# Performance work log

Measured on AMD Instinct MI355X. Metric: run time of the kernel, lower is better.

## Reference

```python
import jax, jax.numpy as jnp
import numpy as np

N_NODES = 512
N_VEC = 8          # n_vectors_hidden
N_FEAT = 128       # n_invariant_feat_hidden
MLP_UNITS = [128, 128]


def _mlp(x, Ws):
    # e3nn-style MLP on scalars: no bias, weights scaled by 1/sqrt(fan_in), silu on every layer
    for W in Ws:
        x = jax.nn.silu(x @ W / jnp.sqrt(jnp.asarray(W.shape[0], x.dtype)))
    return x


def setup_inputs() -> dict:
    key = jax.random.key(0)
    ks = jax.random.split(key, 12)
    d_edge = N_VEC + 2 * N_FEAT  # 264
    inp = {
        "positions": jax.random.normal(ks[0], (N_NODES, N_VEC, 3), jnp.float32),
        "features": jax.random.normal(ks[1], (N_NODES, N_FEAT), jnp.float32),
        # phi_e
        "We1": jax.random.normal(ks[2], (d_edge, MLP_UNITS[0]), jnp.float32),
        "We2": jax.random.normal(ks[3], (MLP_UNITS[0], MLP_UNITS[1]), jnp.float32),
        # phi_x
        "Wx1": jax.random.normal(ks[4], (MLP_UNITS[1], MLP_UNITS[0]), jnp.float32),
        "Wx2": jax.random.normal(ks[5], (MLP_UNITS[0], MLP_UNITS[1]), jnp.float32),
        # phi_inf
        "Winf": jax.random.normal(ks[6], (MLP_UNITS[1], 1), jnp.float32),
        # FullyConnectedTensorProduct weights: [scalar_mul, sh_mul, out_mul]
        "Wtp": jax.random.normal(ks[7], (MLP_UNITS[1], N_VEC, N_VEC), jnp.float32),
        # phi_h + final linear
        "Wh1": jax.random.normal(ks[8], (MLP_UNITS[1] + N_FEAT, MLP_UNITS[0]), jnp.float32),
        "Wh2": jax.random.normal(ks[9], (MLP_UNITS[0], MLP_UNITS[1]), jnp.float32),
        "Wh3": jax.random.normal(ks[10], (MLP_UNITS[1], N_FEAT), jnp.float32),
    }
    return inp


def reference(positions, features, We1, We2, Wx1, Wx2, Winf, Wtp, Wh1, Wh2, Wh3):
    n, V, _ = positions.shape
    # fully-connected edge list (senders sorted, self-loops excluded)
    idx = np.arange(n)
    senders = np.repeat(idx, n - 1)                                  # [E]
    receivers = (senders + np.tile(np.arange(1, n), n)) % n          # [E]

    vectors = positions[senders] - positions[receivers]              # [E,V,3]
    sq = jnp.sum(vectors * vectors, axis=-1)
    lengths = jnp.sqrt(jnp.maximum(sq, 1e-20))                       # safe_norm [E,V]

    edge_feat = jnp.concatenate(
        [lengths, features[senders], features[receivers]], axis=-1)  # [E, V+2F]
    m_ij = _mlp(edge_feat, [We1, We2])                               # [E, U]
    phi_x_out = _mlp(m_ij, [Wx1, Wx2])                               # [E, U]

    unit = vectors / lengths[..., None]                              # [E,V,3]
    sh1 = jnp.sqrt(jnp.asarray(3.0, unit.dtype)) * unit              # ell=1, component norm
    # FCTP: only 0e (x) 1o -> 1o path reaches the n_vectors x 1o output
    U = phi_x_out.shape[-1]
    norm = jnp.sqrt(jnp.asarray(U * V, sh1.dtype))
    out_vec = jnp.einsum('uvw,eu,evk->ewk', Wtp, phi_x_out, sh1) / norm  # [E,W,3]

    vector_per_node = jax.ops.segment_sum(out_vec, senders, num_segments=n)  # [n,W,3]

    e = jax.nn.sigmoid(m_ij @ Winf / jnp.sqrt(jnp.asarray(Winf.shape[0], m_ij.dtype)))  # [E,1]
    m_i = jax.ops.segment_sum(m_ij * e, senders, num_segments=n)     # [n,U]

    h = _mlp(jnp.concatenate([m_i, features], axis=-1), [Wh1, Wh2])
    h = h @ Wh3 / jnp.sqrt(jnp.asarray(Wh3.shape[0], h.dtype))       # final linear -> F
    features_out = h + features                                      # residual_h
    positions_out = positions + vector_per_node
    return positions_out, features_out
```

## Files before the change

kernel.cpp:

```cpp
#include <hip/hip_runtime.h>
#include <math.h>

#define NN   512
#define NV   8
#define CH   32
#define NCHH 8

#define C1 0.06154574548966636f
#define C2 0.08838834764831845f
#define SQRT3 1.7320508075688772f

typedef __attribute__((ext_vector_type(8))) short bf16x8;
typedef __attribute__((ext_vector_type(4))) float f32x4;

#define MFMA16 __builtin_amdgcn_mfma_f32_16x16x32_bf16
#define CVT_PK(dst, a, b) asm("v_cvt_pk_bf16_f32 %0, %1, %2" : "=v"(dst) : "v"(a), "v"(b))

__device__ __forceinline__ float silu_f(float x) {
    float e = __builtin_amdgcn_exp2f(x * -1.442695041f);
    return x * __builtin_amdgcn_rcpf(1.0f + e);
}
__device__ __forceinline__ float sigm_f(float x) {
    float e = __builtin_amdgcn_exp2f(x * -1.442695041f);
    return __builtin_amdgcn_rcpf(1.0f + e);
}
__device__ __forceinline__ short f2bf(float f) {
    unsigned u = __builtin_bit_cast(unsigned, f);
    u = (u + 0x7FFFu + ((u >> 16) & 1u)) >> 16;
    return (short)u;
}
__device__ __forceinline__ float bfhi(unsigned u) {
    return __builtin_bit_cast(float, u & 0xFFFF0000u);
}
__device__ __forceinline__ float bflo(unsigned u) {
    return __builtin_bit_cast(float, u << 16);
}

__device__ __forceinline__ void packW(const float* __restrict__ W,
                                      short* __restrict__ out, int ncols, int ct,
                                      float scale)
{
    int t = threadIdx.x;
    int lane = t & 63, kt = (t >> 6) & 3;
    int g = lane >> 4, c = lane & 15;
    bf16x8 v;
    #pragma unroll
    for (int j = 0; j < 8; ++j)
        v[j] = f2bf(W[(kt * 32 + g * 8 + j) * ncols + ct * 16 + c] * scale);
    *(bf16x8*)(out + (size_t)(ct * 256 + t) * 8) = v;
}

__global__ __launch_bounds__(256)
void k_packall(const float* __restrict__ We2, const float* __restrict__ Wx1,
               const float* __restrict__ Wx2, const float* __restrict__ Wtp,
               const float* __restrict__ We1, const float* __restrict__ feat,
               short* __restrict__ We2p, short* __restrict__ Wx1p,
               short* __restrict__ Wx2p, short* __restrict__ Wtpp,
               short* __restrict__ We1Lp,
               float* __restrict__ FsP, float* __restrict__ FrP)
{
    const int b = blockIdx.x, t = threadIdx.x;
    if (b < 8)  { packW(We2, We2p, 128, b,      C2);       return; }
    if (b < 16) { packW(Wx1, Wx1p, 128, b - 8,  C2);       return; }
    if (b < 24) { packW(Wx2, Wx2p, 128, b - 16, C2);       return; }
    if (b < 28) { packW(Wtp, Wtpp,  64, b - 24, 0.03125f); return; }
    if (b == 28) {
        #pragma unroll
        for (int h = 0; h < 2; ++h) {
            int tt = t + h * 256;
            int ct = tt >> 6, l = tt & 63, g = l >> 4, c = l & 15;
            bf16x8 v = {0,0,0,0,0,0,0,0};
            if (g == 0) {
                #pragma unroll
                for (int j = 0; j < 8; ++j)
                    v[j] = f2bf(We1[j * 128 + ct * 16 + c] * C1);
            }
            *(bf16x8*)(We1Lp + (size_t)tt * 8) = v;
        }
        return;
    }
    __shared__ float sF[256];
    const int n = (b - 29) * 2 + (t >> 7), j = t & 127, hb = t & 128;
    sF[t] = feat[n * 128 + j];
    __syncthreads();
    float a = 0.f, bb = 0.f;
    #pragma unroll 8
    for (int k = 0; k < 128; ++k) {
        float f = sF[hb + k];
        a  = fmaf(f, We1[(8   + k) * 128 + j], a);
        bb = fmaf(f, We1[(136 + k) * 128 + j], bb);
    }
    FsP[n * 128 + j] = a * C1;
    FrP[n * 128 + j] = bb * C1;
}

__device__ __forceinline__ void loadBz(const short* __restrict__ p,
                                       bf16x8 (&B)[2][4], int w, int lane)
{
    int zz = 0; asm volatile("" : "+v"(zz));
    const bf16x8* p8 = (const bf16x8*)p;
    #pragma unroll
    for (int ctl = 0; ctl < 2; ++ctl)
        #pragma unroll
        for (int kt = 0; kt < 4; ++kt)
            B[ctl][kt] = p8[((w * 2 + ctl) * 4 + kt) * 64 + lane + zz];
}

__device__ __forceinline__ void gemm_mfma(const short* sIn_, const bf16x8 (&B)[2][4],
                                          const int (&adrK)[4], f32x4 (&acc)[2][2])
{
    const char* sIn = (const char*)sIn_;
    const f32x4 z = {0.f, 0.f, 0.f, 0.f};
    acc[0][0] = z; acc[0][1] = z; acc[1][0] = z; acc[1][1] = z;
    __builtin_amdgcn_s_setprio(1);
    #pragma unroll
    for (int kt = 0; kt < 4; ++kt) {
        bf16x8 a0 = *(const bf16x8*)(sIn + adrK[kt]);
        bf16x8 a1 = *(const bf16x8*)(sIn + adrK[kt] + 4096);
        acc[0][0] = MFMA16(a0, B[0][kt], acc[0][0], 0, 0, 0);
        acc[0][1] = MFMA16(a0, B[1][kt], acc[0][1], 0, 0, 0);
        acc[1][0] = MFMA16(a1, B[0][kt], acc[1][0], 0, 0, 0);
        acc[1][1] = MFMA16(a1, B[1][kt], acc[1][1], 0, 0, 0);
    }
    __builtin_amdgcn_s_setprio(0);
}

template<bool KEEP>
__device__ __forceinline__ void epi_store(const f32x4 (&acc)[2][2], short* sOut_,
                                          const int (&wAdr)[2][4], f32x4 (&keep)[2][2])
{
    char* sOut = (char*)sOut_;
    #pragma unroll
    for (int rt = 0; rt < 2; ++rt)
        #pragma unroll
        for (int ctl = 0; ctl < 2; ++ctl) {
            float v0 = silu_f(acc[rt][ctl][0]);
            float v1 = silu_f(acc[rt][ctl][1]);
            float v2 = silu_f(acc[rt][ctl][2]);
            float v3 = silu_f(acc[rt][ctl][3]);
            if (KEEP) {
                keep[rt][ctl][0] = v0; keep[rt][ctl][1] = v1;
                keep[rt][ctl][2] = v2; keep[rt][ctl][3] = v3;
            }
            unsigned p01, p23;
            CVT_PK(p01, v0, v1);
            CVT_PK(p23, v2, v3);
            char* o = sOut + rt * 4096;
            *(short*)(o + wAdr[ctl][0]) = (short)(p01 & 0xFFFFu);
            *(short*)(o + wAdr[ctl][1]) = (short)(p01 >> 16);
            *(short*)(o + wAdr[ctl][2]) = (short)(p23 & 0xFFFFu);
            *(short*)(o + wAdr[ctl][3]) = (short)(p23 >> 16);
        }
}

__global__ __launch_bounds__(256, 4)
void k_edge(const float* __restrict__ pos,
            const float* __restrict__ Winf,
            const float* __restrict__ FsP,
            const float* __restrict__ FrP,
            const short* __restrict__ We1Lp,
            const short* __restrict__ We2p,
            const short* __restrict__ Wx1p,
            const short* __restrict__ Wx2p,
            const short* __restrict__ Wtpp,
            float* __restrict__ MI2,
            float* __restrict__ VEC2)
{
    __shared__ __align__(16) short sX[CH * 128];
    __shared__ __align__(16) short sY[CH * 128];
    __shared__ __align__(16) float sLS[CH * NV * 4];
    __shared__ float sWinf[8 * 17];
    __shared__ float sPosS[24];
    __shared__ float sE[CH];
    __shared__ float sVp[4 * 24];

    const int bid = blockIdx.x;
    const int s = bid >> 1, half = bid & 1;
    const int t = threadIdx.x;
    const int lane = t & 63, w = t >> 6;
    const int rl = lane & 15, kg = lane >> 4;

    const int swz = (rl & 7) << 4;
    const int ktperm = (rl & 4) << 4;
    const int baseRd = rl * 256 + ((kg * 16) ^ (swz & 0x30));
    int adrK[4];
    #pragma unroll
    for (int kt = 0; kt < 4; ++kt) adrK[kt] = baseRd + ((kt * 64) ^ ktperm);
    int wAdr[2][4];
    #pragma unroll
    for (int ctl = 0; ctl < 2; ++ctl)
        #pragma unroll
        for (int jj = 0; jj < 4; ++jj) {
            int r = kg * 4 + jj;
            wAdr[ctl][jj] = r * 256 + ((w * 64 + ctl * 32 + 2 * rl) ^ ((r & 7) << 4));
        }
    const int colg0 = w * 32 + rl, colg1 = colg0 + 16;
    const int er = t >> 3, eo = t & 7;
    const int eAdr0 = er * 256 + ((eo * 32)      ^ ((er & 7) << 4));
    const int eAdr1 = er * 256 + ((eo * 32 + 16) ^ ((er & 7) << 4));
    const int vv = w * 2 + (rl >> 3);

    if (t < 128) sWinf[(t >> 4) * 17 + (t & 15)] = Winf[t];
    if (t < 24)  sPosS[t] = pos[s * 24 + t];

    const float fs0 = FsP[s * 128 + colg0];
    const float fs1 = FsP[s * 128 + colg1];

    float miacc0 = 0.f, miacc1 = 0.f;
    float vax = 0.f, vay = 0.f, vaz = 0.f;
    __syncthreads();

    for (int c = 0; c < NCHH; ++c) {
        const int r0 = (half * NCHH + c) * CH;

        bf16x8 Bw[2][4];
        loadBz(We2p, Bw, w, lane);
        bf16x8 bL0, bL1;
        {
            int zz = 0; asm volatile("" : "+v"(zz));
            const bf16x8* pL = (const bf16x8*)We1Lp;
            bL0 = pL[(w * 2 + 0) * 64 + lane + zz];
            bL1 = pL[(w * 2 + 1) * 64 + lane + zz];
        }
        f32x4 cIn[2][2];
        {
            int zz = 0; asm volatile("" : "+v"(zz));
            #pragma unroll
            for (int rt = 0; rt < 2; ++rt)
                #pragma unroll
                for (int jj = 0; jj < 4; ++jj) {
                    const float* fp = FrP + (size_t)(r0 + rt * 16 + kg * 4 + jj) * 128 + zz;
                    cIn[rt][0][jj] = fp[colg0] + fs0;
                    cIn[rt][1][jj] = fp[colg1] + fs1;
                }
        }

        {
            int r = t >> 3, v = t & 7;
            const float* pr = pos + (size_t)(r0 + r) * 24 + v * 3;
            float dx = sPosS[v * 3 + 0] - pr[0];
            float dy = sPosS[v * 3 + 1] - pr[1];
            float dz = sPosS[v * 3 + 2] - pr[2];
            float sq = fmaxf(dx * dx + dy * dy + dz * dz, 1e-20f);
            float rs = __builtin_amdgcn_rsqf(sq);
            float len = sq * rs;
            float inv = SQRT3 * rs;
            f32x4 o; o[0] = dx * inv; o[1] = dy * inv; o[2] = dz * inv; o[3] = len;
            *(f32x4*)(sLS + (r * 8 + (v ^ (r & 7))) * 4) = o;
        }
        __syncthreads();

        {
            bf16x8 aL0 = {0,0,0,0,0,0,0,0}, aL1 = {0,0,0,0,0,0,0,0};
            if (kg == 0) {
                const float* Lp = sLS + rl * 32;
                const float* Lq = sLS + (rl + 16) * 32;
                unsigned u0[4], u1[4];
                #pragma unroll
                for (int jp = 0; jp < 4; ++jp) {
                    CVT_PK(u0[jp], Lp[((2*jp)   ^ (rl & 7)) * 4 + 3],
                                   Lp[((2*jp+1) ^ (rl & 7)) * 4 + 3]);
                    CVT_PK(u1[jp], Lq[((2*jp)   ^ (rl & 7)) * 4 + 3],
                                   Lq[((2*jp+1) ^ (rl & 7)) * 4 + 3]);
                }
                uint4 v0 = {u0[0], u0[1], u0[2], u0[3]};
                uint4 v1 = {u1[0], u1[1], u1[2], u1[3]};
                aL0 = __builtin_bit_cast(bf16x8, v0);
                aL1 = __builtin_bit_cast(bf16x8, v1);
            }
            f32x4 aP[2][2];
            aP[0][0] = MFMA16(aL0, bL0, cIn[0][0], 0, 0, 0);
            aP[0][1] = MFMA16(aL0, bL1, cIn[0][1], 0, 0, 0);
            aP[1][0] = MFMA16(aL1, bL0, cIn[1][0], 0, 0, 0);
            aP[1][1] = MFMA16(aL1, bL1, cIn[1][1], 0, 0, 0);
            f32x4 dummy[2][2];
            epi_store<false>(aP, sX, wAdr, dummy);
        }
        __syncthreads();

        f32x4 acc[2][2];
        f32x4 keepM[2][2];
        gemm_mfma(sX, Bw, adrK, acc);
        bf16x8 Bn[2][4];
        loadBz(Wx1p, Bn, w, lane);
        epi_store<true>(acc, sY, wAdr, keepM);
        __syncthreads();

        {
            const char* sYc = (const char*)sY;
            uint4 m0 = *(const uint4*)(sYc + eAdr0);
            uint4 m1 = *(const uint4*)(sYc + eAdr1);
            const unsigned mu[8] = {m0.x, m0.y, m0.z, m0.w, m1.x, m1.y, m1.z, m1.w};
            float d = 0.f;
            #pragma unroll
            for (int q = 0; q < 8; ++q) {
                d = fmaf(bflo(mu[q]), sWinf[eo * 17 + 2 * q],     d);
                d = fmaf(bfhi(mu[q]), sWinf[eo * 17 + 2 * q + 1], d);
            }
            d += __shfl_xor(d, 1); d += __shfl_xor(d, 2); d += __shfl_xor(d, 4);
            if (eo == 0) sE[er] = (r0 + er == s) ? 0.f : sigm_f(d * C2);
        }
        __syncthreads();

        #pragma unroll
        for (int rt = 0; rt < 2; ++rt)
            #pragma unroll
            for (int jj = 0; jj < 4; ++jj) {
                float e = sE[rt * 16 + kg * 4 + jj];
                miacc0 = fmaf(keepM[rt][0][jj], e, miacc0);
                miacc1 = fmaf(keepM[rt][1][jj], e, miacc1);
            }

        gemm_mfma(sY, Bn, adrK, acc);
        loadBz(Wx2p, Bw, w, lane);
        epi_store<false>(acc, sX, wAdr, keepM);
        __syncthreads();

        gemm_mfma(sX, Bw, adrK, acc);
        bf16x8 Bt[4];
        {
            int zz = 0; asm volatile("" : "+v"(zz));
            const bf16x8* p8 = (const bf16x8*)Wtpp;
            #pragma unroll
            for (int kt = 0; kt < 4; ++kt) Bt[kt] = p8[(w * 4 + kt) * 64 + lane + zz];
        }
        epi_store<false>(acc, sY, wAdr, keepM);
        __syncthreads();

        {
            const f32x4 z = {0.f, 0.f, 0.f, 0.f};
            f32x4 acc0 = z, acc1 = z;
            const char* sYc = (const char*)sY;
            __builtin_amdgcn_s_setprio(1);
            #pragma unroll
            for (int kt = 0; kt < 4; ++kt) {
                bf16x8 a0 = *(const bf16x8*)(sYc + adrK[kt]);
                bf16x8 a1 = *(const bf16x8*)(sYc + adrK[kt] + 4096);
                acc0 = MFMA16(a0, Bt[kt], acc0, 0, 0, 0);
                acc1 = MFMA16(a1, Bt[kt], acc1, 0, 0, 0);
            }
            __builtin_amdgcn_s_setprio(0);
            #pragma unroll
            for (int rt = 0; rt < 2; ++rt)
                #pragma unroll
                for (int jj = 0; jj < 4; ++jj) {
                    int row = rt * 16 + kg * 4 + jj;
                    const f32x4 sh = *(const f32x4*)(sLS + (row * 8 + (vv ^ (row & 7))) * 4);
                    float g = rt ? acc1[jj] : acc0[jj];
                    vax = fmaf(g, sh[0], vax);
                    vay = fmaf(g, sh[1], vay);
                    vaz = fmaf(g, sh[2], vaz);
                }
        }
        __syncthreads();
    }

    miacc0 += __shfl_xor(miacc0, 16); miacc0 += __shfl_xor(miacc0, 32);
    miacc1 += __shfl_xor(miacc1, 16); miacc1 += __shfl_xor(miacc1, 32);
    if (lane < 16) {
        float* mo = MI2 + (size_t)(half * NN + s) * 128;
        mo[w * 32 + lane]      = miacc0;
        mo[w * 32 + 16 + lane] = miacc1;
    }
    vax += __shfl_xor(vax, 8);  vay += __shfl_xor(vay, 8);  vaz += __shfl_xor(vaz, 8);
    vax += __shfl_xor(vax, 16); vay += __shfl_xor(vay, 16); vaz += __shfl_xor(vaz, 16);
    vax += __shfl_xor(vax, 32); vay += __shfl_xor(vay, 32); vaz += __shfl_xor(vaz, 32);
    if ((lane & 56) == 0) {
        float* vp = sVp + w * 24 + lane * 3;
        vp[0] = vax; vp[1] = vay; vp[2] = vaz;
    }
    __syncthreads();
    if (t < 24) {
        float sum = sVp[t] + sVp[24 + t] + sVp[48 + t] + sVp[72 + t];
        VEC2[(size_t)(half * NN + s) * 24 + t] = sum;
    }
}

__global__ __launch_bounds__(128)
void k_node(const float* __restrict__ pos, const float* __restrict__ feat,
            const float* __restrict__ Wh1, const float* __restrict__ Wh2,
            const float* __restrict__ Wh3,
            const float* __restrict__ MI2, const float* __restrict__ VEC2,
            float* __restrict__ outPos, float* __restrict__ outFeat)
{
    __shared__ float sMi[128], sF[128], sH[128];
    int n = blockIdx.x, j = threadIdx.x;
    sMi[j] = MI2[n * 128 + j] + MI2[NN * 128 + n * 128 + j];
    sF[j]  = feat[n * 128 + j];
    __syncthreads();
    float a = 0.f;
    #pragma unroll 8
    for (int k = 0; k < 128; ++k) a = fmaf(sMi[k], Wh1[k * 128 + j], a);
    #pragma unroll 8
    for (int k = 0; k < 128; ++k) a = fmaf(sF[k], Wh1[(128 + k) * 128 + j], a);
    a = silu_f(a * 0.0625f);
    sH[j] = a;
    __syncthreads();
    float b = 0.f;
    #pragma unroll 8
    for (int k = 0; k < 128; ++k) b = fmaf(sH[k], Wh2[k * 128 + j], b);
    b = silu_f(b * C2);
    sMi[j] = b;
    __syncthreads();
    float cc = 0.f;
    #pragma unroll 8
    for (int k = 0; k < 128; ++k) cc = fmaf(sMi[k], Wh3[k * 128 + j], cc);
    outFeat[n * 128 + j] = cc * C2 + sF[j];
    if (j < 24) outPos[n * 24 + j] = pos[n * 24 + j]
                                   + VEC2[n * 24 + j] + VEC2[NN * 24 + n * 24 + j];
}

extern "C" void kernel_launch(void* const* d_in, const int* in_sizes, int n_in,
                              void* d_out, int out_size, void* d_ws, size_t ws_size,
                              hipStream_t stream) {
    const float* pos  = (const float*)d_in[0];
    const float* feat = (const float*)d_in[1];
    const float* We1  = (const float*)d_in[2];
    const float* We2  = (const float*)d_in[3];
    const float* Wx1  = (const float*)d_in[4];
    const float* Wx2  = (const float*)d_in[5];
    const float* Winf = (const float*)d_in[6];
    const float* Wtp  = (const float*)d_in[7];
    const float* Wh1  = (const float*)d_in[8];
    const float* Wh2  = (const float*)d_in[9];
    const float* Wh3  = (const float*)d_in[10];

    float* outPos  = (float*)d_out;
    float* outFeat = (float*)d_out + NN * 24;

    float* ws   = (float*)d_ws;
    float* FsP  = ws;
    float* FrP  = ws + 65536;
    float* MI2  = ws + 131072;
    float* VEC2 = ws + 262144;
    short* wpack = (short*)(ws + 286720);
    short* We2p  = wpack;
    short* Wx1p  = wpack + 16384;
    short* Wx2p  = wpack + 32768;
    short* Wtpp  = wpack + 49152;
    short* We1Lp = wpack + 57344;

    k_packall<<<dim3(285), dim3(256), 0, stream>>>(We2, Wx1, Wx2, Wtp, We1, feat,
                                                   We2p, Wx1p, Wx2p, Wtpp, We1Lp,
                                                   FsP, FrP);
    k_edge<<<dim3(2 * NN), dim3(256), 0, stream>>>(pos, Winf, FsP, FrP, We1Lp,
                                                   We2p, Wx1p, Wx2p, Wtpp, MI2, VEC2);
    k_node<<<dim3(NN), dim3(128), 0, stream>>>(pos, feat, Wh1, Wh2, Wh3, MI2, VEC2,
                                               outPos, outFeat);
}
```

Baseline: 94.97 us.

## Double-buffer edge geometry and prefetch next chunk to drop barriers

Edge geometry (unit vectors and lengths) now sits in a double-buffered shared array. The next chunk's geometry is computed during the current chunk's phi_x stage instead of at the top of each iteration, which removes that iteration's barrier. The first phi_x GEMM and its epilogue move before the barrier that publishes the attention weights, and the barrier at the end of the loop is dropped, leaving fewer block-wide syncs per chunk. The cost is extra shared memory and registers for the sender positions, plus more reliance on the remaining barriers to order the shared-buffer reuse correctly.

```diff
diff --git a/kernel.cpp b/kernel.cpp
--- a/kernel.cpp
+++ b/kernel.cpp
@@ -168,9 +168,8 @@
 {
     __shared__ __align__(16) short sX[CH * 128];
     __shared__ __align__(16) short sY[CH * 128];
-    __shared__ __align__(16) float sLS[CH * NV * 4];
+    __shared__ __align__(16) float sLS[2][CH * NV * 4];
     __shared__ float sWinf[8 * 17];
-    __shared__ float sPosS[24];
     __shared__ float sE[CH];
     __shared__ float sVp[4 * 24];
 
@@ -201,17 +200,36 @@
     const int vv = w * 2 + (rl >> 3);
 
     if (t < 128) sWinf[(t >> 4) * 17 + (t & 15)] = Winf[t];
-    if (t < 24)  sPosS[t] = pos[s * 24 + t];
 
     const float fs0 = FsP[s * 128 + colg0];
     const float fs1 = FsP[s * 128 + colg1];
 
+    const int p0r = t >> 3, p0v = t & 7;
+    const int p0off = (p0r * 8 + (p0v ^ (p0r & 7))) * 4;
+    const float psx = pos[s * 24 + p0v * 3 + 0];
+    const float psy = pos[s * 24 + p0v * 3 + 1];
+    const float psz = pos[s * 24 + p0v * 3 + 2];
+
     float miacc0 = 0.f, miacc1 = 0.f;
     float vax = 0.f, vay = 0.f, vaz = 0.f;
+
+    {
+        int row = ((half * NCHH) * CH + p0r) & 511;
+        const float* pr = pos + (size_t)row * 24 + p0v * 3;
+        float dx = psx - pr[0], dy = psy - pr[1], dz = psz - pr[2];
+        float sq = fmaxf(dx * dx + dy * dy + dz * dz, 1e-20f);
+        float rs = __builtin_amdgcn_rsqf(sq);
+        float len = sq * rs;
+        float inv = SQRT3 * rs;
+        f32x4 o; o[0] = dx * inv; o[1] = dy * inv; o[2] = dz * inv; o[3] = len;
+        *(f32x4*)(sLS[0] + p0off) = o;
+    }
     __syncthreads();
 
     for (int c = 0; c < NCHH; ++c) {
         const int r0 = (half * NCHH + c) * CH;
+        const float* lsCur = sLS[c & 1];
+        float* lsNxt = sLS[(c + 1) & 1];
 
         bf16x8 Bw[2][4];
         loadBz(We2p, Bw, w, lane);
@@ -236,25 +254,10 @@
         }
 
         {
-            int r = t >> 3, v = t & 7;
-            const float* pr = pos + (size_t)(r0 + r) * 24 + v * 3;
-            float dx = sPosS[v * 3 + 0] - pr[0];
-            float dy = sPosS[v * 3 + 1] - pr[1];
-            float dz = sPosS[v * 3 + 2] - pr[2];
-            float sq = fmaxf(dx * dx + dy * dy + dz * dz, 1e-20f);
-            float rs = __builtin_amdgcn_rsqf(sq);
-            float len = sq * rs;
-            float inv = SQRT3 * rs;
-            f32x4 o; o[0] = dx * inv; o[1] = dy * inv; o[2] = dz * inv; o[3] = len;
-            *(f32x4*)(sLS + (r * 8 + (v ^ (r & 7))) * 4) = o;
-        }
-        __syncthreads();
-
-        {
             bf16x8 aL0 = {0,0,0,0,0,0,0,0}, aL1 = {0,0,0,0,0,0,0,0};
             if (kg == 0) {
-                const float* Lp = sLS + rl * 32;
-                const float* Lq = sLS + (rl + 16) * 32;
+                const float* Lp = lsCur + rl * 32;
+                const float* Lq = lsCur + (rl + 16) * 32;
                 unsigned u0[4], u1[4];
                 #pragma unroll
                 for (int jp = 0; jp < 4; ++jp) {
@@ -300,6 +303,10 @@
             d += __shfl_xor(d, 1); d += __shfl_xor(d, 2); d += __shfl_xor(d, 4);
             if (eo == 0) sE[er] = (r0 + er == s) ? 0.f : sigm_f(d * C2);
         }
+
+        gemm_mfma(sY, Bn, adrK, acc);
+        loadBz(Wx2p, Bw, w, lane);
+        epi_store<false>(acc, sX, wAdr, keepM);
         __syncthreads();
 
         #pragma unroll
@@ -311,11 +318,6 @@
                 miacc1 = fmaf(keepM[rt][1][jj], e, miacc1);
             }
 
-        gemm_mfma(sY, Bn, adrK, acc);
-        loadBz(Wx2p, Bw, w, lane);
-        epi_store<false>(acc, sX, wAdr, keepM);
-        __syncthreads();
-
         gemm_mfma(sX, Bw, adrK, acc);
         bf16x8 Bt[4];
         {
@@ -323,6 +325,17 @@
             const bf16x8* p8 = (const bf16x8*)Wtpp;
             #pragma unroll
             for (int kt = 0; kt < 4; ++kt) Bt[kt] = p8[(w * 4 + kt) * 64 + lane + zz];
+        }
+        {
+            int row = (r0 + CH + p0r) & 511;
+            const float* pr = pos + (size_t)row * 24 + p0v * 3;
+            float dx = psx - pr[0], dy = psy - pr[1], dz = psz - pr[2];
+            float sq = fmaxf(dx * dx + dy * dy + dz * dz, 1e-20f);
+            float rs = __builtin_amdgcn_rsqf(sq);
+            float len = sq * rs;
+            float inv = SQRT3 * rs;
+            f32x4 o; o[0] = dx * inv; o[1] = dy * inv; o[2] = dz * inv; o[3] = len;
+            *(f32x4*)(lsNxt + p0off) = o;
         }
         epi_store<false>(acc, sY, wAdr, keepM);
         __syncthreads();
@@ -345,14 +358,13 @@
                 #pragma unroll
                 for (int jj = 0; jj < 4; ++jj) {
                     int row = rt * 16 + kg * 4 + jj;
-                    const f32x4 sh = *(const f32x4*)(sLS + (row * 8 + (vv ^ (row & 7))) * 4);
+                    const f32x4 sh = *(const f32x4*)(lsCur + (row * 8 + (vv ^ (row & 7))) * 4);
                     float g = rt ? acc1[jj] : acc0[jj];
                     vax = fmaf(g, sh[0], vax);
                     vay = fmaf(g, sh[1], vay);
                     vaz = fmaf(g, sh[2], vaz);
                 }
         }
-        __syncthreads();
     }
 
     miacc0 += __shfl_xor(miacc0, 16); miacc0 += __shfl_xor(miacc0, 32);
```

New measurement: 96.52 us. Within noise of the previous version (+1.6%).

## Double edge-kernel block to 512 threads with 16-column tiles per wave

Applied to the files above, without the earlier changes.

The edge kernel now uses 8 waves per block instead of 4. Each wave computes 16 output columns instead of 32, which halves per-thread MFMA accumulators and weight registers. The goal is more waves in flight to hide latency and shorter serial per-wave chains. In exchange there are more barrier participants, each weight fragment is loaded by more waves, and the final TP GEMM runs on only half the waves.

```diff
diff --git a/kernel.cpp b/kernel.cpp
--- a/kernel.cpp
+++ b/kernel.cpp
@@ -94,66 +94,60 @@
     FrP[n * 128 + j] = bb * C1;
 }
 
-__device__ __forceinline__ void loadBz(const short* __restrict__ p,
-                                       bf16x8 (&B)[2][4], int w, int lane)
+__device__ __forceinline__ void loadB16(const short* __restrict__ p,
+                                        bf16x8 (&B)[4], int w, int lane)
 {
     int zz = 0; asm volatile("" : "+v"(zz));
     const bf16x8* p8 = (const bf16x8*)p;
     #pragma unroll
-    for (int ctl = 0; ctl < 2; ++ctl)
-        #pragma unroll
-        for (int kt = 0; kt < 4; ++kt)
-            B[ctl][kt] = p8[((w * 2 + ctl) * 4 + kt) * 64 + lane + zz];
-}
-
-__device__ __forceinline__ void gemm_mfma(const short* sIn_, const bf16x8 (&B)[2][4],
-                                          const int (&adrK)[4], f32x4 (&acc)[2][2])
+    for (int kt = 0; kt < 4; ++kt)
+        B[kt] = p8[(w * 4 + kt) * 64 + lane + zz];
+}
+
+__device__ __forceinline__ void gemm16(const short* sIn_, const bf16x8 (&B)[4],
+                                       const int (&adrK)[4], f32x4 (&acc)[2])
 {
     const char* sIn = (const char*)sIn_;
     const f32x4 z = {0.f, 0.f, 0.f, 0.f};
-    acc[0][0] = z; acc[0][1] = z; acc[1][0] = z; acc[1][1] = z;
+    acc[0] = z; acc[1] = z;
     __builtin_amdgcn_s_setprio(1);
     #pragma unroll
     for (int kt = 0; kt < 4; ++kt) {
         bf16x8 a0 = *(const bf16x8*)(sIn + adrK[kt]);
         bf16x8 a1 = *(const bf16x8*)(sIn + adrK[kt] + 4096);
-        acc[0][0] = MFMA16(a0, B[0][kt], acc[0][0], 0, 0, 0);
-        acc[0][1] = MFMA16(a0, B[1][kt], acc[0][1], 0, 0, 0);
-        acc[1][0] = MFMA16(a1, B[0][kt], acc[1][0], 0, 0, 0);
-        acc[1][1] = MFMA16(a1, B[1][kt], acc[1][1], 0, 0, 0);
+        acc[0] = MFMA16(a0, B[kt], acc[0], 0, 0, 0);
+        acc[1] = MFMA16(a1, B[kt], acc[1], 0, 0, 0);
     }
     __builtin_amdgcn_s_setprio(0);
 }
 
 template<bool KEEP>
-__device__ __forceinline__ void epi_store(const f32x4 (&acc)[2][2], short* sOut_,
-                                          const int (&wAdr)[2][4], f32x4 (&keep)[2][2])
+__device__ __forceinline__ void epi16(const f32x4 (&acc)[2], short* sOut_,
+                                      const int (&wAdr4)[4], f32x4 (&keep)[2])
 {
     char* sOut = (char*)sOut_;
     #pragma unroll
-    for (int rt = 0; rt < 2; ++rt)
-        #pragma unroll
-        for (int ctl = 0; ctl < 2; ++ctl) {
-            float v0 = silu_f(acc[rt][ctl][0]);
-            float v1 = silu_f(acc[rt][ctl][1]);
-            float v2 = silu_f(acc[rt][ctl][2]);
-            float v3 = silu_f(acc[rt][ctl][3]);
-            if (KEEP) {
-                keep[rt][ctl][0] = v0; keep[rt][ctl][1] = v1;
-                keep[rt][ctl][2] = v2; keep[rt][ctl][3] = v3;
-            }
-            unsigned p01, p23;
-            CVT_PK(p01, v0, v1);
-            CVT_PK(p23, v2, v3);
-            char* o = sOut + rt * 4096;
-            *(short*)(o + wAdr[ctl][0]) = (short)(p01 & 0xFFFFu);
-            *(short*)(o + wAdr[ctl][1]) = (short)(p01 >> 16);
-            *(short*)(o + wAdr[ctl][2]) = (short)(p23 & 0xFFFFu);
-            *(short*)(o + wAdr[ctl][3]) = (short)(p23 >> 16);
-        }
-}
-
-__global__ __launch_bounds__(256, 4)
+    for (int rt = 0; rt < 2; ++rt) {
+        float v0 = silu_f(acc[rt][0]);
+        float v1 = silu_f(acc[rt][1]);
+        float v2 = silu_f(acc[rt][2]);
+        float v3 = silu_f(acc[rt][3]);
+        if (KEEP) {
+            keep[rt][0] = v0; keep[rt][1] = v1;
+            keep[rt][2] = v2; keep[rt][3] = v3;
+        }
+        unsigned p01, p23;
+        CVT_PK(p01, v0, v1);
+        CVT_PK(p23, v2, v3);
+        char* o = sOut + rt * 4096;
+        *(short*)(o + wAdr4[0]) = (short)(p01 & 0xFFFFu);
+        *(short*)(o + wAdr4[1]) = (short)(p01 >> 16);
+        *(short*)(o + wAdr4[2]) = (short)(p23 & 0xFFFFu);
+        *(short*)(o + wAdr4[3]) = (short)(p23 >> 16);
+    }
+}
+
+__global__ __launch_bounds__(512, 6)
 void k_edge(const float* __restrict__ pos,
             const float* __restrict__ Winf,
             const float* __restrict__ FsP,
@@ -186,56 +180,41 @@
     int adrK[4];
     #pragma unroll
     for (int kt = 0; kt < 4; ++kt) adrK[kt] = baseRd + ((kt * 64) ^ ktperm);
-    int wAdr[2][4];
-    #pragma unroll
-    for (int ctl = 0; ctl < 2; ++ctl)
-        #pragma unroll
-        for (int jj = 0; jj < 4; ++jj) {
-            int r = kg * 4 + jj;
-            wAdr[ctl][jj] = r * 256 + ((w * 64 + ctl * 32 + 2 * rl) ^ ((r & 7) << 4));
-        }
-    const int colg0 = w * 32 + rl, colg1 = colg0 + 16;
-    const int er = t >> 3, eo = t & 7;
-    const int eAdr0 = er * 256 + ((eo * 32)      ^ ((er & 7) << 4));
-    const int eAdr1 = er * 256 + ((eo * 32 + 16) ^ ((er & 7) << 4));
+    int wAdr4[4];
+    #pragma unroll
+    for (int jj = 0; jj < 4; ++jj) {
+        int r = kg * 4 + jj;
+        wAdr4[jj] = r * 256 + ((w * 32 + 2 * rl) ^ ((r & 7) << 4));
+    }
+    const int colg = w * 16 + rl;
+    const int erow = t >> 4, eseg = t & 15;
+    const int eAdr = erow * 256 + ((eseg * 16) ^ ((erow & 7) << 4));
     const int vv = w * 2 + (rl >> 3);
 
     if (t < 128) sWinf[(t >> 4) * 17 + (t & 15)] = Winf[t];
     if (t < 24)  sPosS[t] = pos[s * 24 + t];
 
-    const float fs0 = FsP[s * 128 + colg0];
-    const float fs1 = FsP[s * 128 + colg1];
-
-    float miacc0 = 0.f, miacc1 = 0.f;
+    const float fs0 = FsP[s * 128 + colg];
+
+    float miacc0 = 0.f;
     float vax = 0.f, vay = 0.f, vaz = 0.f;
     __syncthreads();
 
     for (int c = 0; c < NCHH; ++c) {
         const int r0 = (half * NCHH + c) * CH;
 
-        bf16x8 Bw[2][4];
-        loadBz(We2p, Bw, w, lane);
-        bf16x8 bL0, bL1;
-        {
-            int zz = 0; asm volatile("" : "+v"(zz));
-            const bf16x8* pL = (const bf16x8*)We1Lp;
-            bL0 = pL[(w * 2 + 0) * 64 + lane + zz];
-            bL1 = pL[(w * 2 + 1) * 64 + lane + zz];
-        }
-        f32x4 cIn[2][2];
+        float frv[2][4];
         {
             int zz = 0; asm volatile("" : "+v"(zz));
             #pragma unroll
             for (int rt = 0; rt < 2; ++rt)
                 #pragma unroll
-                for (int jj = 0; jj < 4; ++jj) {
-                    const float* fp = FrP + (size_t)(r0 + rt * 16 + kg * 4 + jj) * 128 + zz;
-                    cIn[rt][0][jj] = fp[colg0] + fs0;
-                    cIn[rt][1][jj] = fp[colg1] + fs1;
-                }
-        }
-
-        {
+                for (int jj = 0; jj < 4; ++jj)
+                    frv[rt][jj] = FrP[(size_t)(r0 + rt * 16 + kg * 4 + jj) * 128 + colg + zz]
+                                + fs0;
+        }
+
+        if (t < 256) {
             int r = t >> 3, v = t & 7;
             const float* pr = pos + (size_t)(r0 + r) * 24 + v * 3;
             float dx = sPosS[v * 3 + 0] - pr[0];
@@ -251,6 +230,11 @@
         __syncthreads();
 
         {
+            bf16x8 bL0;
+            {
+                int zz = 0; asm volatile("" : "+v"(zz));
+                bL0 = ((const bf16x8*)We1Lp)[w * 64 + lane + zz];
+            }
             bf16x8 aL0 = {0,0,0,0,0,0,0,0}, aL1 = {0,0,0,0,0,0,0,0};
             if (kg == 0) {
                 const float* Lp = sLS + rl * 32;
@@ -268,85 +252,73 @@
                 aL0 = __builtin_bit_cast(bf16x8, v0);
                 aL1 = __builtin_bit_cast(bf16x8, v1);
             }
-            f32x4 aP[2][2];
-            aP[0][0] = MFMA16(aL0, bL0, cIn[0][0], 0, 0, 0);
-            aP[0][1] = MFMA16(aL0, bL1, cIn[0][1], 0, 0, 0);
-            aP[1][0] = MFMA16(aL1, bL0, cIn[1][0], 0, 0, 0);
-            aP[1][1] = MFMA16(aL1, bL1, cIn[1][1], 0, 0, 0);
-            f32x4 dummy[2][2];
-            epi_store<false>(aP, sX, wAdr, dummy);
-        }
-        __syncthreads();
-
-        f32x4 acc[2][2];
-        f32x4 keepM[2][2];
-        gemm_mfma(sX, Bw, adrK, acc);
-        bf16x8 Bn[2][4];
-        loadBz(Wx1p, Bn, w, lane);
-        epi_store<true>(acc, sY, wAdr, keepM);
-        __syncthreads();
-
-        {
-            const char* sYc = (const char*)sY;
-            uint4 m0 = *(const uint4*)(sYc + eAdr0);
-            uint4 m1 = *(const uint4*)(sYc + eAdr1);
-            const unsigned mu[8] = {m0.x, m0.y, m0.z, m0.w, m1.x, m1.y, m1.z, m1.w};
+            f32x4 aP[2];
+            aP[0] = MFMA16(aL0, bL0, *(const f32x4*)frv[0], 0, 0, 0);
+            aP[1] = MFMA16(aL1, bL0, *(const f32x4*)frv[1], 0, 0, 0);
+            f32x4 dummy[2];
+            epi16<false>(aP, sX, wAdr4, dummy);
+        }
+        __syncthreads();
+
+        f32x4 acc[2], keepM[2];
+        {
+            bf16x8 B[4];
+            loadB16(We2p, B, w, lane);
+            gemm16(sX, B, adrK, acc);
+            epi16<true>(acc, sY, wAdr4, keepM);
+        }
+        __syncthreads();
+
+        {
+            uint4 m = *(const uint4*)((const char*)sY + eAdr);
+            const unsigned mu[4] = {m.x, m.y, m.z, m.w};
+            const float* wf = sWinf + (eseg >> 1) * 17 + (eseg & 1) * 8;
             float d = 0.f;
             #pragma unroll
-            for (int q = 0; q < 8; ++q) {
-                d = fmaf(bflo(mu[q]), sWinf[eo * 17 + 2 * q],     d);
-                d = fmaf(bfhi(mu[q]), sWinf[eo * 17 + 2 * q + 1], d);
+            for (int i = 0; i < 4; ++i) {
+                d = fmaf(bflo(mu[i]), wf[2 * i],     d);
+                d = fmaf(bfhi(mu[i]), wf[2 * i + 1], d);
             }
-            d += __shfl_xor(d, 1); d += __shfl_xor(d, 2); d += __shfl_xor(d, 4);
-            if (eo == 0) sE[er] = (r0 + er == s) ? 0.f : sigm_f(d * C2);
+            d += __shfl_xor(d, 1); d += __shfl_xor(d, 2);
+            d += __shfl_xor(d, 4); d += __shfl_xor(d, 8);
+            if (eseg == 0) sE[erow] = (r0 + erow == s) ? 0.f : sigm_f(d * C2);
         }
         __syncthreads();
 
         #pragma unroll
         for (int rt = 0; rt < 2; ++rt)
             #pragma unroll
-            for (int jj = 0; jj < 4; ++jj) {
-                float e = sE[rt * 16 + kg * 4 + jj];
-                miacc0 = fmaf(keepM[rt][0][jj], e, miacc0);
-                miacc1 = fmaf(keepM[rt][1][jj], e, miacc1);
-            }
-
-        gemm_mfma(sY, Bn, adrK, acc);
-        loadBz(Wx2p, Bw, w, lane);
-        epi_store<false>(acc, sX, wAdr, keepM);
-        __syncthreads();
-
-        gemm_mfma(sX, Bw, adrK, acc);
-        bf16x8 Bt[4];
-        {
-            int zz = 0; asm volatile("" : "+v"(zz));
-            const bf16x8* p8 = (const bf16x8*)Wtpp;
-            #pragma unroll
-            for (int kt = 0; kt < 4; ++kt) Bt[kt] = p8[(w * 4 + kt) * 64 + lane + zz];
-        }
-        epi_store<false>(acc, sY, wAdr, keepM);
-        __syncthreads();
-
-        {
-            const f32x4 z = {0.f, 0.f, 0.f, 0.f};
-            f32x4 acc0 = z, acc1 = z;
-            const char* sYc = (const char*)sY;
-            __builtin_amdgcn_s_setprio(1);
-            #pragma unroll
-            for (int kt = 0; kt < 4; ++kt) {
-                bf16x8 a0 = *(const bf16x8*)(sYc + adrK[kt]);
-                bf16x8 a1 = *(const bf16x8*)(sYc + adrK[kt] + 4096);
-                acc0 = MFMA16(a0, Bt[kt], acc0, 0, 0, 0);
-                acc1 = MFMA16(a1, Bt[kt], acc1, 0, 0, 0);
-            }
-            __builtin_amdgcn_s_setprio(0);
+            for (int jj = 0; jj < 4; ++jj)
+                miacc0 = fmaf(keepM[rt][jj], sE[rt * 16 + kg * 4 + jj], miacc0);
+
+        {
+            bf16x8 B[4];
+            loadB16(Wx1p, B, w, lane);
+            gemm16(sY, B, adrK, acc);
+            epi16<false>(acc, sX, wAdr4, keepM);
+        }
+        __syncthreads();
+
+        {
+            bf16x8 B[4];
+            loadB16(Wx2p, B, w, lane);
+            gemm16(sX, B, adrK, acc);
+            epi16<false>(acc, sY, wAdr4, keepM);
+        }
+        __syncthreads();
+
+        if (w < 4) {
+            bf16x8 Bt[4];
+            loadB16(Wtpp, Bt, w, lane);
+            f32x4 a2[2];
+            gemm16(sY, Bt, adrK, a2);
             #pragma unroll
             for (int rt = 0; rt < 2; ++rt)
                 #pragma unroll
                 for (int jj = 0; jj < 4; ++jj) {
                     int row = rt * 16 + kg * 4 + jj;
                     const f32x4 sh = *(const f32x4*)(sLS + (row * 8 + (vv ^ (row & 7))) * 4);
-                    float g = rt ? acc1[jj] : acc0[jj];
+                    float g = a2[rt][jj];
                     vax = fmaf(g, sh[0], vax);
                     vay = fmaf(g, sh[1], vay);
                     vaz = fmaf(g, sh[2], vaz);
@@ -356,18 +328,17 @@
     }
 
     miacc0 += __shfl_xor(miacc0, 16); miacc0 += __shfl_xor(miacc0, 32);
-    miacc1 += __shfl_xor(miacc1, 16); miacc1 += __shfl_xor(miacc1, 32);
     if (lane < 16) {
-        float* mo = MI2 + (size_t)(half * NN + s) * 128;
-        mo[w * 32 + lane]      = miacc0;
-        mo[w * 32 + 16 + lane] = miacc1;
-    }
-    vax += __shfl_xor(vax, 8);  vay += __shfl_xor(vay, 8);  vaz += __shfl_xor(vaz, 8);
-    vax += __shfl_xor(vax, 16); vay += __shfl_xor(vay, 16); vaz += __shfl_xor(vaz, 16);
-    vax += __shfl_xor(vax, 32); vay += __shfl_xor(vay, 32); vaz += __shfl_xor(vaz, 32);
-    if ((lane & 56) == 0) {
-        float* vp = sVp + w * 24 + lane * 3;
-        vp[0] = vax; vp[1] = vay; vp[2] = vaz;
+        MI2[(size_t)(half * NN + s) * 128 + w * 16 + lane] = miacc0;
+    }
+    if (w < 4) {
+        vax += __shfl_xor(vax, 8);  vay += __shfl_xor(vay, 8);  vaz += __shfl_xor(vaz, 8);
+        vax += __shfl_xor(vax, 16); vay += __shfl_xor(vay, 16); vaz += __shfl_xor(vaz, 16);
+        vax += __shfl_xor(vax, 32); vay += __shfl_xor(vay, 32); vaz += __shfl_xor(vaz, 32);
+        if ((lane & 56) == 0) {
+            float* vp = sVp + w * 24 + lane * 3;
+            vp[0] = vax; vp[1] = vay; vp[2] = vaz;
+        }
     }
     __syncthreads();
     if (t < 24) {
@@ -443,7 +414,7 @@
     k_packall<<<dim3(285), dim3(256), 0, stream>>>(We2, Wx1, Wx2, Wtp, We1, feat,
                                                    We2p, Wx1p, Wx2p, Wtpp, We1Lp,
                                                    FsP, FrP);
-    k_edge<<<dim3(2 * NN), dim3(256), 0, stream>>>(pos, Winf, FsP, FrP, We1Lp,
+    k_edge<<<dim3(2 * NN), dim3(512), 0, stream>>>(pos, Winf, FsP, FrP, We1Lp,
                                                    We2p, Wx1p, Wx2p, Wtpp, MI2, VEC2);
     k_node<<<dim3(NN), dim3(128), 0, stream>>>(pos, feat, Wh1, Wh2, Wh3, MI2, VEC2,
                                                outPos, outFeat);
```

Result: slower. 128.2 us (+35.0%).
